# Kernel optimization log

Measured on AMD Instinct MI355X. Metric: run time of the kernel, lower is better.

The kernel has to match this reference:

```python
import jax, jax.numpy as jnp
import numpy as np

DIM = 256


def _layernorm(x, g, b, eps=1e-5):
    mu = x.mean(-1, keepdims=True)
    var = x.var(-1, keepdims=True)  # biased, matches torch LayerNorm
    return (x - mu) / jnp.sqrt(var + eps) * g + b


def _softmax_kernel(d, proj, ratio, eps=1e-4):
    # FAVOR+ softmax kernel feature map: ratio*(exp(d@proj^T - |d|^2/2) + eps)
    dd = jnp.einsum('bnc,fc->bnf', d, proj)
    diag = 0.5 * jnp.sum(d * d, axis=-1, keepdims=True)
    return ratio * (jnp.exp(dd - diag) + eps)


def setup_inputs() -> dict:
    d = DIM
    rng = np.random.default_rng(0)
    # gaussian orthogonal random matrix (nb_features == dim -> single QR block)
    qmat, _ = np.linalg.qr(rng.standard_normal((d, d)))
    mult = np.linalg.norm(rng.standard_normal((d, d)), axis=1)
    proj = (np.diag(mult) @ qmat.T).astype(np.float32)

    key = jax.random.key(0)
    ks = jax.random.split(key, 8)

    def lin(k, o, i):
        s = 1.0 / np.sqrt(i)
        return jax.random.uniform(k, (o, i), jnp.float32, -s, s)

    return {
        'x': jax.random.normal(ks[0], (8, d, 64, 64), jnp.float32),
        'proj': jnp.asarray(proj),
        'wq': lin(ks[1], d, d), 'bq': jnp.zeros((d,), jnp.float32),
        'wk': lin(ks[2], d, d), 'bk': jnp.zeros((d,), jnp.float32),
        'wa': lin(ks[3], d, d), 'ba': jnp.zeros((d,), jnp.float32),
        'g1': jnp.ones((d,), jnp.float32), 'b1': jnp.zeros((d,), jnp.float32),
        'g2': jnp.ones((d,), jnp.float32), 'b2': jnp.zeros((d,), jnp.float32),
        'w1': lin(ks[4], 4 * d, d), 'fb1': jnp.zeros((4 * d,), jnp.float32),
        'w2': lin(ks[5], d, 4 * d), 'fb2': jnp.zeros((d,), jnp.float32),
    }


def reference(x, proj, wq, bq, wk, bk, wa, ba, g1, b1, g2, b2, w1, fb1, w2, fb2):
    B, C, H, W = x.shape
    N = H * W
    t = x.reshape(B, C, N).transpose(0, 2, 1)  # [B, N, C] tokens
    shortcut = t
    h = _layernorm(t, g1, b1)
    # 1x1 convs == per-token linears (conv weight [out,in,1,1] -> [out,in])
    q = h @ wq.T + bq
    k = h @ wk.T + bk
    v = h @ wa.T + ba
    # F.normalize(p=2, dim=channel, eps=5e-5): x / max(||x||, eps)
    qn = q / jnp.maximum(jnp.linalg.norm(q, axis=-1, keepdims=True), 5e-5)
    kn = k / jnp.maximum(jnp.linalg.norm(k, axis=-1, keepdims=True), 5e-5)
    ratio = proj.shape[0] ** -0.5
    qp = _softmax_kernel(qn, proj, ratio)  # [B, N, F]
    kp = _softmax_kernel(kn, proj, ratio)  # [B, N, F]
    # linear attention (single head, squeezed)
    k_sum = kp.sum(axis=1)                                    # [B, F]
    D_inv = 1.0 / jnp.einsum('bnf,bf->bn', qp, k_sum)         # [B, N]
    ctx = jnp.einsum('bnf,bnc->bfc', kp, v)                   # [B, F, C]
    out = jnp.einsum('bfc,bnf,bn->bnc', ctx, qp, D_inv)       # [B, N, C]
    t = shortcut + out
    h2 = _layernorm(t, g2, b2)
    m = jax.nn.gelu(h2 @ w1.T + fb1, approximate=False) @ w2.T + fb2
    t = t + m
    return t.transpose(0, 2, 1).reshape(B, C, H, W)
```

## Files before the change

### kernel.cpp

```cpp
#include <hip/hip_runtime.h>
#include <hip/hip_bf16.h>
#include <math.h>

typedef __hip_bfloat16 bf16;
typedef __attribute__((ext_vector_type(8))) short short8;
typedef __attribute__((ext_vector_type(4))) short short4v;
typedef __attribute__((ext_vector_type(4))) unsigned short ushort4v;
typedef __attribute__((ext_vector_type(4))) float f32x4;
typedef unsigned int u32;

#define BB 8
#define CC 256
#define NTOKB 4096
#define FF 256
#define HIDDEN 1024
#define NTOK (BB*NTOKB)

#if defined(__has_builtin)
#if __has_builtin(__builtin_amdgcn_global_load_lds)
#define HAS_GLL 1
#endif
#endif
#ifndef HAS_GLL
#define HAS_GLL 0
#endif

__device__ __forceinline__ float bf2f(bf16 x) { return __bfloat162float(x); }
__device__ __forceinline__ bf16 f2bf(float x) { return __float2bfloat16(x); }
__device__ __forceinline__ float clampf(float v, float lo, float hi) {
    return fminf(fmaxf(v, lo), hi);
}
__device__ __forceinline__ float s2f(short s) {
    unsigned int u = ((unsigned int)(unsigned short)s) << 16;
    float f; __builtin_memcpy(&f, &u, 4); return f;
}
__device__ __forceinline__ unsigned short f2bits(float v) {
    bf16 h = f2bf(v);
    unsigned short b; __builtin_memcpy(&b, &h, 2); return b;
}

#if HAS_GLL
__device__ __forceinline__ void gll16(const void* g, void* l) {
    __builtin_amdgcn_global_load_lds(
        (const __attribute__((address_space(1))) u32*)g,
        (__attribute__((address_space(3))) u32*)l, 16, 0, 0);
}
#endif

__device__ __forceinline__ float ldin(const void* p, size_t i, int fp32mode) {
    float v = fp32mode ? ((const float*)p)[i] : __bfloat162float(((const bf16*)p)[i]);
    if (!(v == v)) v = 0.f;
    return clampf(v, -1e4f, 1e4f);
}

__device__ __forceinline__ float wave_sum(float v) {
#pragma unroll
    for (int off = 32; off > 0; off >>= 1) v += __shfl_xor(v, off, 64);
    return v;
}

__global__ void detect_mode(const void* __restrict__ x, int* __restrict__ flag) {
    int i = threadIdx.x;
    float vb = __bfloat162float(((const bf16*)x)[(size_t)i * 37 + 1]);
    int bad = (!(vb == vb)) || (fabsf(vb) > 1e4f);
    unsigned long long m = __ballot(bad);
    if (i == 0) *flag = (m != 0ull) ? 1 : 0;
}

__global__ void convw_all(const void* __restrict__ wq, const void* __restrict__ wk,
                          const void* __restrict__ wa, const void* __restrict__ proj,
                          const void* __restrict__ w1, const void* __restrict__ w2,
                          const void* __restrict__ bq, const void* __restrict__ bk,
                          const void* __restrict__ ba,
                          bf16* __restrict__ dst, float* __restrict__ bqkv,
                          const int* __restrict__ mode) {
    int fp32 = *mode;
    int i = blockIdx.x * 256 + threadIdx.x;
    if (i < 786432) {
        const void* src; size_t off;
        if (i < 262144) {
            int seg = i >> 16; off = (size_t)(i & 65535);
            src = seg == 0 ? wq : seg == 1 ? wk : seg == 2 ? wa : proj;
        } else if (i < 524288) { src = w1; off = (size_t)(i - 262144); }
        else { src = w2; off = (size_t)(i - 524288); }
        dst[i] = f2bf(ldin(src, off, fp32));
    } else if (i < 787200) {
        int j = i - 786432;
        const void* s = j < 256 ? bq : j < 512 ? bk : ba;
        bqkv[j] = ldin(s, (size_t)(j & 255), fp32);
    }
}


__global__ void transpose_in_off(const void* __restrict__ X, bf16* __restrict__ T,
                                 const int* __restrict__ mode, size_t eoff) {
    __shared__ float tile[32][33];
    int fp32 = *mode;
    int n0 = blockIdx.x * 32, c0 = blockIdx.y * 32;
    int tx = threadIdx.x, ty = threadIdx.y;
    for (int i = ty; i < 32; i += 8)
        tile[i][tx] = ldin(X, eoff + (size_t)(c0 + i) * NTOKB + n0 + tx, fp32);
    __syncthreads();
    for (int i = ty; i < 32; i += 8)
        T[(size_t)(n0 + i) * CC + c0 + tx] = f2bf(tile[tx][i]);
}

__global__ void transpose_out_off(const bf16* __restrict__ T, void* __restrict__ O,
                                  const int* __restrict__ mode, size_t eoff) {
    __shared__ float tile[32][33];
    int fp32 = *mode;
    int c0 = blockIdx.x * 32, n0 = blockIdx.y * 32;
    int tx = threadIdx.x, ty = threadIdx.y;
    for (int i = ty; i < 32; i += 8)
        tile[i][tx] = bf2f(T[(size_t)(n0 + i) * CC + c0 + tx]);
    __syncthreads();
    for (int i = ty; i < 32; i += 8) {
        size_t idx = eoff + (size_t)(c0 + i) * NTOKB + n0 + tx;
        float v = tile[tx][i];
        if (fp32) ((float*)O)[idx] = v; else ((bf16*)O)[idx] = f2bf(v);
    }
}

__global__ void transpose_in_z(const void* __restrict__ X, bf16* __restrict__ T,
                               const int* __restrict__ mode) {
    __shared__ float tile[32][33];
    int fp32 = *mode;
    int b = blockIdx.z;
    int n0 = blockIdx.x * 32, c0 = blockIdx.y * 32;
    int tx = threadIdx.x, ty = threadIdx.y;
    size_t eoff = (size_t)b * CC * NTOKB;
    for (int i = ty; i < 32; i += 8)
        tile[i][tx] = ldin(X, eoff + (size_t)(c0 + i) * NTOKB + n0 + tx, fp32);
    __syncthreads();
    for (int i = ty; i < 32; i += 8)
        T[((size_t)b * NTOKB + n0 + i) * CC + c0 + tx] = f2bf(tile[tx][i]);
}

__global__ void transpose_out_z(const bf16* __restrict__ T, void* __restrict__ O,
                                const int* __restrict__ mode) {
    __shared__ float tile[32][33];
    int fp32 = *mode;
    int b = blockIdx.z;
    int c0 = blockIdx.x * 32, n0 = blockIdx.y * 32;
    int tx = threadIdx.x, ty = threadIdx.y;
    for (int i = ty; i < 32; i += 8)
        tile[i][tx] = bf2f(T[((size_t)b * NTOKB + n0 + i) * CC + c0 + tx]);
    __syncthreads();
    for (int i = ty; i < 32; i += 8) {
        size_t idx = (size_t)b * CC * NTOKB + (size_t)(c0 + i) * NTOKB + n0 + tx;
        float v = tile[tx][i];
        if (fp32) ((float*)O)[idx] = v; else ((bf16*)O)[idx] = f2bf(v);
    }
}

__global__ void layernorm_k(const bf16* __restrict__ X, const void* __restrict__ g,
                            const void* __restrict__ bta, bf16* __restrict__ Y,
                            const int* __restrict__ mode) {
    int fp32 = *mode;
    int t = blockIdx.x * 4 + (threadIdx.x >> 6);
    int lane = threadIdx.x & 63;
    const bf16* row = X + (size_t)t * CC;
    float v[4], s = 0.f, s2 = 0.f;
#pragma unroll
    for (int j = 0; j < 4; j++) {
        v[j] = bf2f(row[lane + 64 * j]);
        s += v[j]; s2 += v[j] * v[j];
    }
    s = wave_sum(s); s2 = wave_sum(s2);
    float mu = s * (1.f / CC);
    float var = s2 * (1.f / CC) - mu * mu;
    float rstd = rsqrtf(fmaxf(var, 0.f) + 1e-5f);
    bf16* yrow = Y + (size_t)t * CC;
#pragma unroll
    for (int j = 0; j < 4; j++) {
        int c = lane + 64 * j;
        yrow[c] = f2bf((v[j] - mu) * rstd * ldin(g, c, fp32) + ldin(bta, c, fp32));
    }
}

__global__ void layernorm_v(const bf16* __restrict__ X, const void* __restrict__ g,
                            const void* __restrict__ bta, bf16* __restrict__ Y,
                            const int* __restrict__ mode) {
    int fp32 = *mode;
    int t = blockIdx.x * 4 + (threadIdx.x >> 6);
    int lane = threadIdx.x & 63;
    const short* row = (const short*)X + (size_t)t * CC;
    short4v u = *(const short4v*)&row[lane * 4];
    float v[4], s = 0.f, s2 = 0.f;
#pragma unroll
    for (int j = 0; j < 4; j++) { v[j] = s2f(u[j]); s += v[j]; s2 += v[j] * v[j]; }
    s = wave_sum(s); s2 = wave_sum(s2);
    float mu = s * (1.f / CC);
    float var = s2 * (1.f / CC) - mu * mu;
    float rstd = rsqrtf(fmaxf(var, 0.f) + 1e-5f);
    ushort4v o;
#pragma unroll
    for (int j = 0; j < 4; j++) {
        int c = lane * 4 + j;
        o[j] = f2bits((v[j] - mu) * rstd * ldin(g, c, fp32) + ldin(bta, c, fp32));
    }
    *(ushort4v*)((unsigned short*)Y + (size_t)t * CC + lane * 4) = o;
}

__global__ void rownorm_k(bf16* __restrict__ Q, float* __restrict__ DIAG) {
    int t = blockIdx.x * 4 + (threadIdx.x >> 6);
    int lane = threadIdx.x & 63;
    bf16* row = Q + (size_t)t * CC;
    float v[4], s2 = 0.f;
#pragma unroll
    for (int j = 0; j < 4; j++) { v[j] = bf2f(row[lane + 64 * j]); s2 += v[j] * v[j]; }
    s2 = wave_sum(s2);
    float nrm = sqrtf(fmaxf(s2, 0.f));
    float scale = 1.f / fmaxf(nrm, 5e-5f);
#pragma unroll
    for (int j = 0; j < 4; j++) row[lane + 64 * j] = f2bf(v[j] * scale);
    if (lane == 0) DIAG[t] = 0.5f * s2 * scale * scale;
}

__global__ void rownorm_v(bf16* __restrict__ Q, float* __restrict__ DIAG) {
    int t = blockIdx.x * 4 + (threadIdx.x >> 6);
    int lane = threadIdx.x & 63;
    short* row = (short*)Q + (size_t)t * CC;
    short4v u = *(const short4v*)&row[lane * 4];
    float v[4], s2 = 0.f;
#pragma unroll
    for (int j = 0; j < 4; j++) { v[j] = s2f(u[j]); s2 += v[j] * v[j]; }
    s2 = wave_sum(s2);
    float nrm = sqrtf(fmaxf(s2, 0.f));
    float scale = 1.f / fmaxf(nrm, 5e-5f);
    ushort4v o;
#pragma unroll
    for (int j = 0; j < 4; j++) o[j] = f2bits(v[j] * scale);
    *(ushort4v*)&row[lane * 4] = o;
    if (lane == 0) DIAG[t] = 0.5f * s2 * scale * scale;
}


template <int EPI>
__global__ void gemm_nt(const bf16* __restrict__ A, const void* __restrict__ Bw,
                        const void* __restrict__ bias, const float* __restrict__ diag,
                        const bf16* __restrict__ resid, bf16* __restrict__ Cm,
                        int M, int Nn, int Kk, const int* __restrict__ mode) {
    __shared__ float As[32][33];
    __shared__ float Bs[32][33];
    int fp32 = *mode;
    int tx = threadIdx.x, ty = threadIdx.y;
    int n0 = blockIdx.x * 32, m0 = blockIdx.y * 32;
    int tid = ty * 16 + tx;
    int lr = tid >> 5, lc = tid & 31;
    float acc[2][2] = {{0.f, 0.f}, {0.f, 0.f}};
    for (int k0 = 0; k0 < Kk; k0 += 32) {
#pragma unroll
        for (int i = 0; i < 4; i++) {
            int r = lr + 8 * i;
            As[r][lc] = bf2f(A[(size_t)(m0 + r) * Kk + k0 + lc]);
            Bs[r][lc] = ldin(Bw, (size_t)(n0 + r) * Kk + k0 + lc, fp32);
        }
        __syncthreads();
#pragma unroll
        for (int kk = 0; kk < 32; kk++) {
            float a0 = As[ty][kk], a1 = As[ty + 16][kk];
            float b0 = Bs[tx][kk], b1 = Bs[tx + 16][kk];
            acc[0][0] += a0 * b0; acc[0][1] += a0 * b1;
            acc[1][0] += a1 * b0; acc[1][1] += a1 * b1;
        }
        __syncthreads();
    }
#pragma unroll
    for (int i = 0; i < 2; i++)
#pragma unroll
        for (int j = 0; j < 2; j++) {
            int m = m0 + ty + 16 * i, n = n0 + tx + 16 * j;
            float v = acc[i][j];
            if (EPI == 0) {
                v = clampf(v + ldin(bias, n, fp32), -1e6f, 1e6f);
            } else if (EPI == 1) {
                v = fminf(0.0625f * (expf(fminf(v - diag[m], 60.f)) + 1e-4f), 1e8f);
            } else if (EPI == 2) {
                v += ldin(bias, n, fp32);
                v = 0.5f * v * (1.f + erff(v * 0.70710678118654752f));
            } else if (EPI == 3) {
                v += ldin(bias, n, fp32);
                v = clampf(v + bf2f(resid[(size_t)m * Nn + n]), -1e6f, 1e6f);
            }
            Cm[(size_t)m * Nn + n] = f2bf(v);
        }
}

__global__ void gemm_ctx_fb(const bf16* __restrict__ KP, const bf16* __restrict__ V,
                            float* __restrict__ CTX) {
    __shared__ float Ks[32][33];
    __shared__ float Vs[32][33];
    int c0 = blockIdx.x * 32, f0 = blockIdx.y * 32;
    int tx = threadIdx.x, ty = threadIdx.y;
    int tid = ty * 16 + tx, lr = tid >> 5, lc = tid & 31;
    float acc[2][2] = {{0.f, 0.f}, {0.f, 0.f}};
    for (int n0 = 0; n0 < NTOKB; n0 += 32) {
#pragma unroll
        for (int i = 0; i < 4; i++) {
            int r = lr + 8 * i;
            Ks[r][lc] = bf2f(KP[(size_t)(n0 + r) * FF + f0 + lc]);
            Vs[r][lc] = bf2f(V[(size_t)(n0 + r) * CC + c0 + lc]);
        }
        __syncthreads();
#pragma unroll
        for (int kk = 0; kk < 32; kk++) {
            float a0 = Ks[kk][ty], a1 = Ks[kk][ty + 16];
            float b0 = Vs[kk][tx], b1 = Vs[kk][tx + 16];
            acc[0][0] += a0 * b0; acc[0][1] += a0 * b1;
            acc[1][0] += a1 * b0; acc[1][1] += a1 * b1;
        }
        __syncthreads();
    }
#pragma unroll
    for (int i = 0; i < 2; i++)
#pragma unroll
        for (int j = 0; j < 2; j++)
            CTX[(size_t)(f0 + ty + 16 * i) * CC + c0 + tx + 16 * j] =
                clampf(acc[i][j], -1e18f, 1e18f);
}

__global__ void gemm_attnout_fb(const bf16* __restrict__ QP, const float* __restrict__ CTX,
                                const float* __restrict__ DINV, bf16* __restrict__ T) {
    __shared__ float As[32][33];
    __shared__ float Bs[32][33];
    int c0 = blockIdx.x * 32, m0 = blockIdx.y * 32;
    int tx = threadIdx.x, ty = threadIdx.y;
    int tid = ty * 16 + tx, lr = tid >> 5, lc = tid & 31;
    float acc[2][2] = {{0.f, 0.f}, {0.f, 0.f}};
    for (int k0 = 0; k0 < FF; k0 += 32) {
#pragma unroll
        for (int i = 0; i < 4; i++) {
            int r = lr + 8 * i;
            As[r][lc] = bf2f(QP[(size_t)(m0 + r) * FF + k0 + lc]);
            Bs[r][lc] = CTX[(size_t)(k0 + r) * CC + c0 + lc];
        }
        __syncthreads();
#pragma unroll
        for (int kk = 0; kk < 32; kk++) {
            float a0 = As[ty][kk], a1 = As[ty + 16][kk];
            float b0 = Bs[kk][tx], b1 = Bs[kk][tx + 16];
            acc[0][0] += a0 * b0; acc[0][1] += a0 * b1;
            acc[1][0] += a1 * b0; acc[1][1] += a1 * b1;
        }
        __syncthreads();
    }
#pragma unroll
    for (int i = 0; i < 2; i++)
#pragma unroll
        for (int j = 0; j < 2; j++) {
            int t = m0 + ty + 16 * i;
            size_t idx = (size_t)t * CC + c0 + tx + 16 * j;
            float addv = clampf(acc[i][j] * DINV[t], -1e6f, 1e6f);
            T[idx] = f2bf(bf2f(T[idx]) + addv);
        }
}

__global__ void colsum_k(const bf16* __restrict__ KP, float* __restrict__ KPART) {
    int chunk = blockIdx.x;
    int f = threadIdx.x;
    const bf16* base = KP + (size_t)chunk * 128 * FF + f;
    float acc = 0.f;
    for (int i = 0; i < 128; i++) acc += bf2f(base[(size_t)i * FF]);
    KPART[(size_t)chunk * FF + f] = acc;
}

__global__ void ksum_reduce(const float* __restrict__ KPART, float* __restrict__ KSUM) {
    int f = threadIdx.x;
    float acc = 0.f;
#pragma unroll
    for (int c = 0; c < 32; c++) acc += KPART[(size_t)c * FF + f];
    KSUM[f] = acc;
}

__global__ void dinv_k(const bf16* __restrict__ QP, const float* __restrict__ KSUM,
                       float* __restrict__ DINV) {
    int t = blockIdx.x * 4 + (threadIdx.x >> 6);
    int lane = threadIdx.x & 63;
    const bf16* row = QP + (size_t)t * FF;
    float s = 0.f;
#pragma unroll
    for (int j = 0; j < 4; j++) { int c = lane + 64 * j; s += bf2f(row[c]) * KSUM[c]; }
    s = wave_sum(s);
    if (lane == 0) DINV[t] = fminf(1.f / fmaxf(s, 1e-30f), 1e6f);
}

template <int BM, int BN, int EPI, bool TRANSC>
__global__ __launch_bounds__(256) void mgemm(
    const bf16* __restrict__ A, int lda, long long aZ,
    const void* __restrict__ Bv, int ldb, long long bZ,
    const void* __restrict__ bias, const float* __restrict__ diag,
    const float* __restrict__ dinv,
    bf16* __restrict__ Cb, int ldc,
    bf16* __restrict__ Cb2, bf16* __restrict__ Cb3, float* __restrict__ Cf,
    int MperZ, int Kc, int nchunk, const int* __restrict__ mode)
{
    constexpr int MI = BM / 32;
    constexpr int NI = BN / 32;
    __shared__ short As[BM][32];
    __shared__ short Bs[BN][32];
    int fp32 = *mode;
    int z = blockIdx.z;
    int bl = z / nchunk;
    int chunk = z - bl * nchunk;
    const short* Ag = (const short*)A + (size_t)bl * aZ;
    const short* Bg = (const short*)Bv + (size_t)bl * bZ;

    int bx = blockIdx.x, by = blockIdx.y;
    if ((gridDim.y & 7) == 0) {
        int NB = gridDim.x;
        int flat = by * NB + bx;
        int grp = flat / (8 * NB);
        int rem = flat - grp * 8 * NB;
        by = grp * 8 + (rem & 7);
        bx = rem >> 3;
    }
    int n0 = bx * BN, m0 = by * BM;

    int tid = threadIdx.x;
    int lane = tid & 63, wave = tid >> 6;
    int wm = wave >> 1, wn = wave & 1;
    int row16 = lane & 15, quad = lane >> 4;
    int lrow = lane >> 2, lcol = (lane & 3) * 8;

    f32x4 acc[MI][NI];
#pragma unroll
    for (int i = 0; i < MI; i++)
#pragma unroll
        for (int j = 0; j < NI; j++) acc[i][j] = {0.f, 0.f, 0.f, 0.f};

    int kBase = chunk * Kc;
    for (int kb = kBase; kb < kBase + Kc; kb += 32) {
#pragma unroll
        for (int t = 0; t < BM / 64; t++) {
            int rbase = wave * (BM / 4) + t * 16;
            const short* gsrc = &Ag[(size_t)(m0 + rbase + lrow) * lda + kb + lcol];
#if HAS_GLL
            gll16(gsrc, &As[rbase][0]);
#else
            *(short8*)&As[rbase + lrow][lcol] = *(const short8*)gsrc;
#endif
        }
#pragma unroll
        for (int t = 0; t < BN / 64; t++) {
            int rbase = wave * (BN / 4) + t * 16;
            const short* gsrc = &Bg[(size_t)(n0 + rbase + lrow) * ldb + kb + lcol];
#if HAS_GLL
            gll16(gsrc, &Bs[rbase][0]);
#else
            *(short8*)&Bs[rbase + lrow][lcol] = *(const short8*)gsrc;
#endif
        }
        __syncthreads();
        short8 af[MI], bfr[NI];
#pragma unroll
        for (int i = 0; i < MI; i++)
            af[i] = *(const short8*)&As[wm * (BM / 2) + i * 16 + row16][quad * 8];
#pragma unroll
        for (int j = 0; j < NI; j++)
            bfr[j] = *(const short8*)&Bs[wn * (BN / 2) + j * 16 + row16][quad * 8];
#pragma unroll
        for (int i = 0; i < MI; i++)
#pragma unroll
            for (int j = 0; j < NI; j++)
                acc[i][j] = __builtin_amdgcn_mfma_f32_16x16x32_bf16(af[i], bfr[j], acc[i][j], 0, 0, 0);
        __syncthreads();
    }

    float bv[NI];
    if (EPI == 0 || EPI == 2 || EPI == 3) {
#pragma unroll
        for (int j = 0; j < NI; j++)
            bv[j] = ldin(bias, n0 + wn * (BN / 2) + j * 16 + row16, fp32);
    } else if (EPI == 6) {
#pragma unroll
        for (int j = 0; j < NI; j++)
            bv[j] = diag[n0 + wn * (BN / 2) + j * 16 + row16];
    } else {
#pragma unroll
        for (int j = 0; j < NI; j++) bv[j] = 0.f;
    }

#pragma unroll
    for (int i = 0; i < MI; i++) {
        int mb = m0 + wm * (BM / 2) + i * 16 + quad * 4;
        float dg[4] = {0.f, 0.f, 0.f, 0.f};
        if (EPI == 1) {
#pragma unroll
            for (int r = 0; r < 4; r++) dg[r] = diag[mb + r];
        }
        if (EPI == 7) {
#pragma unroll
            for (int r = 0; r < 4; r++) dg[r] = diag[(size_t)bl * MperZ + mb + r];
        }
        float dvv[4] = {0.f, 0.f, 0.f, 0.f};
        if (EPI == 5) {
#pragma unroll
            for (int r = 0; r < 4; r++) dvv[r] = dinv[(size_t)bl * MperZ + mb + r];
        }
#pragma unroll
        for (int j = 0; j < NI; j++) {
            int n = n0 + wn * (BN / 2) + j * 16 + row16;
            if (EPI == 6) {
                int seg = n0 >> 8;
                int c = n & 255;
                if (seg == 2) {
                    ushort4v pack;
#pragma unroll
                    for (int r = 0; r < 4; r++)
                        pack[r] = f2bits(clampf(acc[i][j][r] + bv[j], -1e6f, 1e6f));
                    int blq = mb >> 12, tb = mb & 4095;
                    *(ushort4v*)((unsigned short*)Cb3 +
                        (size_t)blq * CC * NTOKB + (size_t)c * NTOKB + tb) = pack;
                } else {
                    bf16* dst = seg ? Cb2 : Cb;
#pragma unroll
                    for (int r = 0; r < 4; r++) {
                        float v = clampf(acc[i][j][r] + bv[j], -1e6f, 1e6f);
                        dst[(size_t)(mb + r) * CC + c] = f2bf(v);
                    }
                }
            } else if (EPI == 7) {
                if (bl == 1) {
                    ushort4v pack;
#pragma unroll
                    for (int r = 0; r < 4; r++) {
                        float v = fminf(0.0625f * (expf(fminf(acc[i][j][r] - dg[r], 60.f)) + 1e-4f), 1e8f);
                        pack[r] = f2bits(v);
                    }
                    int blq = mb >> 12, tb = mb & 4095;
                    *(ushort4v*)((unsigned short*)Cb2 +
                        (size_t)blq * CC * NTOKB + (size_t)n * NTOKB + tb) = pack;
                } else {
#pragma unroll
                    for (int r = 0; r < 4; r++) {
                        float v = fminf(0.0625f * (expf(fminf(acc[i][j][r] - dg[r], 60.f)) + 1e-4f), 1e8f);
                        Cb[(size_t)(mb + r) * ldc + n] = f2bf(v);
                    }
                }
            } else if (TRANSC) {
                ushort4v pack;
#pragma unroll
                for (int r = 0; r < 4; r++) {
                    float v = acc[i][j][r];
                    if (EPI == 0) {
                        v = clampf(v + bv[j], -1e6f, 1e6f);
                    } else {
                        v = fminf(0.0625f * (expf(fminf(v - dg[r], 60.f)) + 1e-4f), 1e8f);
                    }
                    pack[r] = f2bits(v);
                }
                int blq = mb >> 12, tb = mb & 4095;
                *(ushort4v*)((unsigned short*)Cb +
                    (size_t)blq * CC * NTOKB + (size_t)n * NTOKB + tb) = pack;
            } else {
#pragma unroll
                for (int r = 0; r < 4; r++) {
                    int m = mb + r;
                    float v = acc[i][j][r];
                    if (EPI == 0) {
                        v = clampf(v + bv[j], -1e6f, 1e6f);
                        Cb[(size_t)m * ldc + n] = f2bf(v);
                    } else if (EPI == 1) {
                        v = fminf(0.0625f * (expf(fminf(v - dg[r], 60.f)) + 1e-4f), 1e8f);
                        Cb[(size_t)m * ldc + n] = f2bf(v);
                    } else if (EPI == 2) {
                        v += bv[j];
                        v = 0.5f * v * (1.f + erff(v * 0.70710678118654752f));
                        Cb[(size_t)m * ldc + n] = f2bf(v);
                    } else if (EPI == 3) {
                        v += bv[j];
                        size_t idx = (size_t)m * ldc + n;
                        v = clampf(v + bf2f(Cb[idx]), -1e6f, 1e6f);
                        Cb[idx] = f2bf(v);
                    } else if (EPI == 4) {
                        Cf[(size_t)z * MperZ + (size_t)m * ldc + n] = v;
                    } else if (EPI == 5) {
                        size_t mg = (size_t)bl * MperZ + m;
                        float addv = clampf(v * dvv[r], -1e6f, 1e6f);
                        size_t idx = mg * ldc + n;
                        Cb[idx] = f2bf(bf2f(Cb[idx]) + addv);
                    }
                }
            }
        }
    }
}

__global__ void reduce_ctx(const float* __restrict__ PART, bf16* __restrict__ CTXT) {
    int f = blockIdx.x;
    int bl = blockIdx.y;
    int c = threadIdx.x;
    float s = 0.f;
#pragma unroll
    for (int ch = 0; ch < 16; ch++)
        s += PART[(((size_t)bl * 16 + ch) * FF + f) * CC + c];
    s = clampf(s, -1e18f, 1e18f);
    CTXT[((size_t)bl * CC + c) * FF + f] = f2bf(s);
}

__global__ void colsum_t(const bf16* __restrict__ KPT, float* __restrict__ KSUM) {
    int bl = blockIdx.y;
    int f = blockIdx.x * 4 + (threadIdx.x >> 6);
    int lane = threadIdx.x & 63;
    const short* row = (const short*)KPT + ((size_t)bl * FF + f) * NTOKB;
    float s = 0.f;
    for (int i = lane * 8; i < NTOKB; i += 512) {
        short8 v = *(const short8*)&row[i];
#pragma unroll
        for (int j = 0; j < 8; j++) s += s2f(v[j]);
    }
    s = wave_sum(s);
    if (lane == 0) KSUM[(size_t)bl * FF + f] = s;
}

__global__ void dinv_v(const bf16* __restrict__ QP, const float* __restrict__ KSUM,
                       float* __restrict__ DINV) {
    int bl = blockIdx.y;
    int t = blockIdx.x * 4 + (threadIdx.x >> 6);
    int lane = threadIdx.x & 63;
    const short* row = (const short*)QP + ((size_t)bl * NTOKB + t) * FF;
    const float* ks = KSUM + (size_t)bl * FF;
    short4v u = *(const short4v*)&row[lane * 4];
    float s = 0.f;
#pragma unroll
    for (int j = 0; j < 4; j++) s += s2f(u[j]) * ks[lane * 4 + j];
    s = wave_sum(s);
    if (lane == 0) DINV[(size_t)bl * NTOKB + t] = fminf(1.f / fmaxf(s, 1e-30f), 1e6f);
}

extern "C" void kernel_launch(void* const* d_in, const int* in_sizes, int n_in,
                              void* d_out, int out_size, void* d_ws, size_t ws_size,
                              hipStream_t stream) {
    const void* x    = d_in[0];
    const void* proj = d_in[1];
    const void* wq   = d_in[2];
    const void* bq   = d_in[3];
    const void* wk   = d_in[4];
    const void* bk   = d_in[5];
    const void* wa   = d_in[6];
    const void* ba   = d_in[7];
    const void* g1   = d_in[8];
    const void* b1   = d_in[9];
    const void* g2   = d_in[10];
    const void* b2   = d_in[11];
    const void* w1   = d_in[12];
    const void* fb1  = d_in[13];
    const void* w2   = d_in[14];
    const void* fb2  = d_in[15];

    char* base = (char*)d_ws;
    const size_t MB = 1048576ull;
    const bool fast = ws_size >= 168 * MB;

    if (fast) {
        bf16* T    = (bf16*)base;
        bf16* Hs   = (bf16*)(base + 16 * MB);
        bf16* Qs   = (bf16*)(base + 32 * MB);
        bf16* Ks   = (bf16*)(base + 48 * MB);
        bf16* VT   = (bf16*)(base + 64 * MB);
        bf16* KPT  = (bf16*)(base + 80 * MB);
        bf16* MID  = (bf16*)(base + 96 * MB);
        float* PART = (float*)(base + 96 * MB);
        char* sm = base + 160 * MB;
        int* MODE = (int*)sm;
        float* DIAGQ = (float*)(sm + 1024);
        float* DIAGK = DIAGQ + NTOK;
        float* DINV  = DIAGK + NTOK;
        float* KSUM  = DINV + NTOK;
        bf16* CTXT   = (bf16*)(sm + 2 * MB);
        bf16* WB     = (bf16*)(sm + 4 * MB);
        float* BQKV  = (float*)(sm + 6 * MB);

        dim3 tb32(32, 8);
        detect_mode<<<1, 64, 0, stream>>>(x, MODE);
        convw_all<<<3075, 256, 0, stream>>>(wq, wk, wa, proj, w1, w2,
                                            bq, bk, ba, WB, BQKV, MODE);
        transpose_in_z<<<dim3(NTOKB / 32, CC / 32, BB), tb32, 0, stream>>>(x, T, MODE);

        layernorm_v<<<NTOK / 4, 256, 0, stream>>>(T, g1, b1, Hs, MODE);
        mgemm<128, 128, 6, false><<<dim3(6, 256, 1), 256, 0, stream>>>(
            Hs, 256, 0, WB, 256, 0, nullptr, BQKV, nullptr,
            Qs, 256, Ks, VT, nullptr, 0, 256, 1, MODE);
        rownorm_v<<<NTOK / 4, 256, 0, stream>>>(Qs, DIAGQ);
        rownorm_v<<<NTOK / 4, 256, 0, stream>>>(Ks, DIAGK);
        mgemm<128, 128, 7, false><<<dim3(2, 256, 2), 256, 0, stream>>>(
            Qs, 256, 8388608LL , WB + 196608, 256, 0,
            nullptr, DIAGQ, nullptr,
            Hs, 256, KPT, nullptr, nullptr, NTOK, 256, 1, MODE);
        bf16* QP = Hs;
        colsum_t<<<dim3(FF / 4, BB), 256, 0, stream>>>(KPT, KSUM);
        dinv_v<<<dim3(NTOKB / 4, BB), 256, 0, stream>>>(QP, KSUM, DINV);
        mgemm<64, 128, 4, false><<<dim3(2, 4, BB * 16), 256, 0, stream>>>(
            KPT, NTOKB, (long long)FF * NTOKB, VT, NTOKB, (long long)CC * NTOKB,
            nullptr, nullptr, nullptr,
            nullptr, CC, nullptr, nullptr, PART, FF * CC, 256, 16, MODE);
        reduce_ctx<<<dim3(FF, BB), 256, 0, stream>>>(PART, CTXT);
        mgemm<128, 64, 5, false><<<dim3(4, 32, BB), 256, 0, stream>>>(
            QP, 256, (long long)NTOKB * FF, CTXT, FF, (long long)CC * FF,
            nullptr, nullptr, DINV,
            T, 256, nullptr, nullptr, nullptr, NTOKB, 256, 1, MODE);
        layernorm_v<<<NTOK / 4, 256, 0, stream>>>(T, g2, b2, Hs, MODE);
        mgemm<128, 128, 2, false><<<dim3(8, 256, 1), 256, 0, stream>>>(
            Hs, 256, 0, WB + 262144, 256, 0, fb1, nullptr, nullptr,
            MID, 1024, nullptr, nullptr, nullptr, 0, 256, 1, MODE);
        mgemm<128, 128, 3, false><<<dim3(2, 256, 1), 256, 0, stream>>>(
            MID, 1024, 0, WB + 524288, 1024, 0, fb2, nullptr, nullptr,
            T, 256, nullptr, nullptr, nullptr, 0, 1024, 1, MODE);
        transpose_out_z<<<dim3(CC / 32, NTOKB / 32, BB), tb32, 0, stream>>>(T, d_out, MODE);
        return;
    }

    bf16* Tb   = (bf16*)(base);
    bf16* Hb   = (bf16*)(base + 2 * MB);
    bf16* Qb   = (bf16*)(base + 4 * MB);
    bf16* Kb   = (bf16*)(base + 6 * MB);
    bf16* Vb   = (bf16*)(base + 8 * MB);
    bf16* QPb  = (bf16*)(base + 2 * MB);
    bf16* KPb  = (bf16*)(base + 4 * MB);
    bf16* MIDb = (bf16*)(base + 2 * MB);
    bf16* H2b  = (bf16*)(base + 10 * MB);
    char* sm   = base + 12 * MB;
    int*   MODE  = (int*)sm;
    float* DIAGQ = (float*)(sm + 256);
    float* DIAGK = DIAGQ + NTOKB;
    float* DINV  = DIAGK + NTOKB;
    float* KSUM  = DINV + NTOKB;
    float* KPART = KSUM + FF;
    float* CTX   = KPART + 32 * FF;

    dim3 tb32(32, 8);
    dim3 tb16(16, 16);
    dim3 gq(CC / 32, NTOKB / 32);

    detect_mode<<<1, 64, 0, stream>>>(x, MODE);

    for (int b = 0; b < BB; b++) {
        size_t eoff = (size_t)b * CC * NTOKB;
        transpose_in_off<<<dim3(NTOKB / 32, CC / 32), tb32, 0, stream>>>(x, Tb, MODE, eoff);
        layernorm_k<<<NTOKB / 4, 256, 0, stream>>>(Tb, g1, b1, Hb, MODE);
        gemm_nt<0><<<gq, tb16, 0, stream>>>(Hb, wq, bq, nullptr, nullptr, Qb, NTOKB, CC, CC, MODE);
        gemm_nt<0><<<gq, tb16, 0, stream>>>(Hb, wk, bk, nullptr, nullptr, Kb, NTOKB, CC, CC, MODE);
        gemm_nt<0><<<gq, tb16, 0, stream>>>(Hb, wa, ba, nullptr, nullptr, Vb, NTOKB, CC, CC, MODE);
        rownorm_k<<<NTOKB / 4, 256, 0, stream>>>(Qb, DIAGQ);
        rownorm_k<<<NTOKB / 4, 256, 0, stream>>>(Kb, DIAGK);
        gemm_nt<1><<<gq, tb16, 0, stream>>>(Qb, proj, nullptr, DIAGQ, nullptr, QPb, NTOKB, FF, CC, MODE);
        gemm_nt<1><<<gq, tb16, 0, stream>>>(Kb, proj, nullptr, DIAGK, nullptr, KPb, NTOKB, FF, CC, MODE);
        colsum_k<<<32, 256, 0, stream>>>(KPb, KPART);
        ksum_reduce<<<1, 256, 0, stream>>>(KPART, KSUM);
        dinv_k<<<NTOKB / 4, 256, 0, stream>>>(QPb, KSUM, DINV);
        gemm_ctx_fb<<<dim3(CC / 32, FF / 32), tb16, 0, stream>>>(KPb, Vb, CTX);
        gemm_attnout_fb<<<gq, tb16, 0, stream>>>(QPb, CTX, DINV, Tb);
        layernorm_k<<<NTOKB / 4, 256, 0, stream>>>(Tb, g2, b2, H2b, MODE);
        gemm_nt<2><<<dim3(HIDDEN / 32, NTOKB / 32), tb16, 0, stream>>>(H2b, w1, fb1, nullptr, nullptr, MIDb, NTOKB, HIDDEN, CC, MODE);
        gemm_nt<3><<<gq, tb16, 0, stream>>>(MIDb, w2, fb2, nullptr, Tb, Tb, NTOKB, CC, HIDDEN, MODE);
        transpose_out_off<<<dim3(CC / 32, NTOKB / 32), tb32, 0, stream>>>(Tb, d_out, MODE, eoff);
    }
}
```

Baseline: 409.5 us.

## Double-buffer LDS tiles in mgemm to overlap global loads with MFMA

Doubles the shared-memory tiles for A and B and restructures the K loop so the next tile is staged into the alternate buffer while MFMAs run on the current one. This cuts one of the two barriers per K step and hides global-to-LDS latency behind compute. It doubles LDS use per block, which may lower occupancy, and correctness depends on the async global_load_lds writes finishing before the single barrier.

```diff
diff --git a/kernel.cpp b/kernel.cpp
--- a/kernel.cpp
+++ b/kernel.cpp
@@ -397,8 +397,8 @@
 {
     constexpr int MI = BM / 32;
     constexpr int NI = BN / 32;
-    __shared__ short As[BM][32];
-    __shared__ short Bs[BN][32];
+    __shared__ short As[2][BM][32];
+    __shared__ short Bs[2][BN][32];
     int fp32 = *mode;
     int z = blockIdx.z;
     int bl = z / nchunk;
@@ -429,43 +429,61 @@
 #pragma unroll
         for (int j = 0; j < NI; j++) acc[i][j] = {0.f, 0.f, 0.f, 0.f};
 
+    const int arb = wave * (BM / 4);
+    const int brb = wave * (BN / 4);
+
     int kBase = chunk * Kc;
-    for (int kb = kBase; kb < kBase + Kc; kb += 32) {
+    int nt = Kc >> 5;
+
+    auto stage = [&](int b, int kb) {
 #pragma unroll
         for (int t = 0; t < BM / 64; t++) {
-            int rbase = wave * (BM / 4) + t * 16;
+            int rbase = arb + t * 16;
             const short* gsrc = &Ag[(size_t)(m0 + rbase + lrow) * lda + kb + lcol];
 #if HAS_GLL
-            gll16(gsrc, &As[rbase][0]);
+            gll16(gsrc, &As[b][rbase][0]);
 #else
-            *(short8*)&As[rbase + lrow][lcol] = *(const short8*)gsrc;
+            *(short8*)&As[b][rbase + lrow][lcol] = *(const short8*)gsrc;
 #endif
         }
 #pragma unroll
         for (int t = 0; t < BN / 64; t++) {
-            int rbase = wave * (BN / 4) + t * 16;
+            int rbase = brb + t * 16;
             const short* gsrc = &Bg[(size_t)(n0 + rbase + lrow) * ldb + kb + lcol];
 #if HAS_GLL
-            gll16(gsrc, &Bs[rbase][0]);
+            gll16(gsrc, &Bs[b][rbase][0]);
 #else
-            *(short8*)&Bs[rbase + lrow][lcol] = *(const short8*)gsrc;
+            *(short8*)&Bs[b][rbase + lrow][lcol] = *(const short8*)gsrc;
 #endif
         }
-        __syncthreads();
+    };
+
+    auto compute = [&](int b) {
         short8 af[MI], bfr[NI];
 #pragma unroll
         for (int i = 0; i < MI; i++)
-            af[i] = *(const short8*)&As[wm * (BM / 2) + i * 16 + row16][quad * 8];
+            af[i] = *(const short8*)&As[b][wm * (BM / 2) + i * 16 + row16][quad * 8];
 #pragma unroll
         for (int j = 0; j < NI; j++)
-            bfr[j] = *(const short8*)&Bs[wn * (BN / 2) + j * 16 + row16][quad * 8];
+            bfr[j] = *(const short8*)&Bs[b][wn * (BN / 2) + j * 16 + row16][quad * 8];
 #pragma unroll
         for (int i = 0; i < MI; i++)
 #pragma unroll
             for (int j = 0; j < NI; j++)
                 acc[i][j] = __builtin_amdgcn_mfma_f32_16x16x32_bf16(af[i], bfr[j], acc[i][j], 0, 0, 0);
+    };
+
+    stage(0, kBase);
+    __syncthreads();
+
+    int cur = 0;
+    for (int t = 0; t + 1 < nt; ++t) {
+        stage(cur ^ 1, kBase + (t + 1) * 32);
+        compute(cur);
         __syncthreads();
-    }
+        cur ^= 1;
+    }
+    compute(cur);
 
     float bv[NI];
     if (EPI == 0 || EPI == 2 || EPI == 3) {
```

Result: no change. 407.2 us (-0.6%).
